# Performance work log

Measured on AMD Instinct MI355X. Metric: run time of the kernel, lower is better.

## Reference

```python
import jax, jax.numpy as jnp
import numpy as np

B, S, D, H = 2, 2048, 256, 8
W_STD = 0.02


def setup_inputs() -> dict:
    key = jax.random.key(0)
    ks = jax.random.split(key, 6)
    x = jax.random.normal(ks[0], (B, S, D), jnp.float32)
    e = jax.random.normal(ks[1], (B, S, D), jnp.float32)
    p = jax.random.normal(ks[2], (B, S, D), jnp.float32)
    W_q = W_STD * jax.random.normal(ks[3], (D, D), jnp.float32)
    W_k = W_STD * jax.random.normal(ks[4], (D, D), jnp.float32)
    W_v = W_STD * jax.random.normal(ks[5], (D, D), jnp.float32)
    gamma = jnp.ones((H, 1, 1), jnp.float32)
    return {"x": x, "e": e, "p": p, "W_q": W_q, "W_k": W_k, "W_v": W_v, "gamma": gamma}


def reference(x, e, p, W_q, W_k, W_v, gamma):
    # use_ppe=True: Q = K = p (broadcast to every head), V = e; each head sees
    # the SAME d_embed-wide copy, so project once and broadcast over heads.
    Q = p @ W_q  # [B,S,D]
    K = p @ W_k  # [B,S,D]
    V = e @ W_v  # [B,S,D]
    # squared euclidean distance (torch.cdist(...,p=2)**2), shared across heads
    q2 = jnp.sum(Q * Q, axis=-1)  # [B,S]
    k2 = jnp.sum(K * K, axis=-1)  # [B,S]
    d2 = q2[:, :, None] + k2[:, None, :] - 2.0 * jnp.einsum('bsd,btd->bst', Q, K)
    d2 = jnp.maximum(d2, 0.0)  # [B,S,S]
    # rbf kernel, per-head gamma: krn = exp(-d2 / (-2*gamma + 1e-6))
    krn = -d2[:, None, :, :] / (-2.0 * gamma + 1e-6)  # [B,H,S,S]
    causal = jnp.tril(jnp.ones((S, S), dtype=bool))  # True where attending allowed
    krn = jnp.where(causal, krn, -jnp.inf)
    krn = jnp.exp(krn)  # masked entries -> exp(-inf) = 0
    # dropout layers run in eval mode (identity)
    out = jnp.einsum('bhst,btd->bhsd', krn, V)  # [B,H,S,D]
    return out
```

## Files before the change

kernel.cpp:

```cpp
#include <hip/hip_runtime.h>
#include <hip/hip_bf16.h>


#define BB   2
#define SS   2048
#define DD   256
#define HH   8
#define BSR  (BB*SS)
#define TSPLIT 4

typedef __bf16 bf16_t;
typedef __bf16 bf16x8 __attribute__((ext_vector_type(8)));
typedef float  f32x4  __attribute__((ext_vector_type(4)));

static __device__ __forceinline__ f32x4 mfma16(bf16x8 a, bf16x8 b, f32x4 c) {
    return __builtin_amdgcn_mfma_f32_16x16x32_bf16(a, b, c, 0, 0, 0);
}

__global__ __launch_bounds__(256) void att_wtrans(
    const float* __restrict__ Wq, const float* __restrict__ Wk,
    const float* __restrict__ Wv,
    bf16_t* __restrict__ WFq_h, bf16_t* __restrict__ WFq_l,
    bf16_t* __restrict__ WFk_h, bf16_t* __restrict__ WFk_l,
    bf16_t* __restrict__ WFv, float* __restrict__ q2, float* __restrict__ k2)
{
    __shared__ float tT[64][68];
    const int tid = threadIdx.x;
    if (blockIdx.x == 48) {
        for (int i = tid; i < BSR; i += 256) { q2[i] = 0.f; k2[i] = 0.f; }
        return;
    }
    const int mat = blockIdx.x >> 4;
    const int tl  = blockIdx.x & 15;
    const int tr  = (tl >> 2) * 64, tc = (tl & 3) * 64;
    const float* W = (mat == 0) ? Wq : ((mat == 1) ? Wk : Wv);

#pragma unroll
    for (int i = 0; i < 4; ++i) {
        const int fidx = i * 256 + tid;
        const int r  = fidx >> 4;
        const int c4 = fidx & 15;
        const float4 v = *(const float4*)(W + (size_t)(tr + r) * DD + tc + c4 * 4);
        tT[c4 * 4 + 0][r] = v.x; tT[c4 * 4 + 1][r] = v.y;
        tT[c4 * 4 + 2][r] = v.z; tT[c4 * 4 + 3][r] = v.w;
    }
    __syncthreads();

#pragma unroll
    for (int i = 0; i < 2; ++i) {
        const int uidx  = i * 256 + tid;
        const int chunk = uidx >> 6;
        const int kc_l  = chunk >> 2, c16 = chunk & 3;
        const int u = uidx & 63, m16 = u & 15, quad = u >> 4;
        const float* src = &tT[c16 * 16 + m16][kc_l * 32 + quad * 8];
        const float4 a = *(const float4*)src;
        const float4 bq = *(const float4*)(src + 4);
        const float f[8] = {a.x, a.y, a.z, a.w, bq.x, bq.y, bq.z, bq.w};
        bf16x8 hi, lo;
#pragma unroll
        for (int j = 0; j < 8; ++j) {
            const bf16_t h = (bf16_t)f[j];
            hi[j] = h; lo[j] = (bf16_t)(f[j] - (float)h);
        }
        const int g16 = (tc >> 4) + c16;
        const int kcg = (tr >> 5) + kc_l;
        const size_t off = ((size_t)(g16 * 8 + kcg)) * 512 + (size_t)u * 8;
        if (mat == 0)      { *(bf16x8*)(WFq_h + off) = hi; *(bf16x8*)(WFq_l + off) = lo; }
        else if (mat == 1) { *(bf16x8*)(WFk_h + off) = hi; *(bf16x8*)(WFk_l + off) = lo; }
        else               { *(bf16x8*)(WFv + off)  = hi; }
    }
}

__global__ __launch_bounds__(256, 2) void att_gemm_qkv(
    const float* __restrict__ p, const float* __restrict__ e,
    const bf16_t* __restrict__ WFq_h, const bf16_t* __restrict__ WFq_l,
    const bf16_t* __restrict__ WFk_h, const bf16_t* __restrict__ WFk_l,
    const bf16_t* __restrict__ WFv,
    bf16_t* __restrict__ QFh, bf16_t* __restrict__ QFl,
    bf16_t* __restrict__ KFh, bf16_t* __restrict__ KFl,
    bf16_t* __restrict__ VF, float* __restrict__ q2, float* __restrict__ k2)
{
    __shared__ float pL[16][264];
    __shared__ float eL[16][264];
    __shared__ float fQ[16][68];
    __shared__ float fK[16][68];
    __shared__ float fV[16][68];

    const int tid  = threadIdx.x;
    const int w    = tid >> 6;
    const int lane = tid & 63;
    const int m16  = lane & 15;
    const int quad = lane >> 4;
    const int row0 = (blockIdx.x >> 2) * 16;
    const int nb   = blockIdx.x & 3;

#pragma unroll
    for (int i = 0; i < 4; ++i) {
        const int fidx = i * 256 + tid;
        const int r  = fidx >> 6;
        const int c4 = fidx & 63;
        const float4 pv = *(const float4*)(p + (size_t)(row0 + r) * DD + c4 * 4);
        const float4 ev = *(const float4*)(e + (size_t)(row0 + r) * DD + c4 * 4);
        *(float4*)&pL[r][c4 * 4] = pv;
        *(float4*)&eL[r][c4 * 4] = ev;
    }
    __syncthreads();

    f32x4 aQ = f32x4{0.f, 0.f, 0.f, 0.f};
    f32x4 aK = f32x4{0.f, 0.f, 0.f, 0.f};
    f32x4 aV = f32x4{0.f, 0.f, 0.f, 0.f};

#pragma unroll 2
    for (int kc = 0; kc < 8; ++kc) {
        const float* ps = &pL[m16][kc * 32 + quad * 8];
        const float* es = &eL[m16][kc * 32 + quad * 8];
        const float4 p0 = *(const float4*)ps;
        const float4 p1 = *(const float4*)(ps + 4);
        const float4 e0 = *(const float4*)es;
        const float4 e1 = *(const float4*)(es + 4);
        const float pa[8] = {p0.x, p0.y, p0.z, p0.w, p1.x, p1.y, p1.z, p1.w};
        const float ea[8] = {e0.x, e0.y, e0.z, e0.w, e1.x, e1.y, e1.z, e1.w};
        bf16x8 aph, apl, aeb;
#pragma unroll
        for (int j = 0; j < 8; ++j) {
            const bf16_t h = (bf16_t)pa[j];
            aph[j] = h;
            apl[j] = (bf16_t)(pa[j] - (float)h);
            aeb[j] = (bf16_t)ea[j];
        }
        const size_t wo = ((size_t)((nb * 4 + w) * 8 + kc)) * 512 + (size_t)lane * 8;
        const bf16x8 bqh = *(const bf16x8*)(WFq_h + wo);
        const bf16x8 bql = *(const bf16x8*)(WFq_l + wo);
        const bf16x8 bkh = *(const bf16x8*)(WFk_h + wo);
        const bf16x8 bkl = *(const bf16x8*)(WFk_l + wo);
        const bf16x8 bv  = *(const bf16x8*)(WFv + wo);
        aQ = mfma16(aph, bqh, aQ);
        aQ = mfma16(apl, bqh, aQ);
        aQ = mfma16(aph, bql, aQ);
        aK = mfma16(aph, bkh, aK);
        aK = mfma16(apl, bkh, aK);
        aK = mfma16(aph, bkl, aK);
        aV = mfma16(aeb, bv, aV);
    }

#pragma unroll
    for (int r = 0; r < 4; ++r) {
        const int rl = quad * 4 + r;
        fQ[rl][w * 16 + m16] = aQ[r];
        fK[rl][w * 16 + m16] = aK[r];
        fV[rl][w * 16 + m16] = aV[r];
    }

#pragma unroll
    for (int r = 0; r < 4; ++r) {
        float vq = aQ[r] * aQ[r], vk = aK[r] * aK[r];
#pragma unroll
        for (int off = 8; off >= 1; off >>= 1) {
            vq += __shfl_xor(vq, off);
            vk += __shfl_xor(vk, off);
        }
        if (m16 == 0) {
            atomicAdd(q2 + row0 + quad * 4 + r, vq);
            atomicAdd(k2 + row0 + quad * 4 + r, vk);
        }
    }

    __syncthreads();

    const int b   = row0 >> 11;
    const int sl  = row0 & 2047;
    const int tt  = sl >> 6;
    const int st  = sl >> 5;
    const int w4  = (sl >> 4) & 3;
    const int mt  = (sl >> 4) & 1;
    const int kc2 = (sl >> 5) & 1;
    const int uh  = (sl >> 4) & 1;

    if (w < 2) {
        const int cl = w;
        const float* src = &fQ[m16][cl * 32 + quad * 8];
        const float4 a = *(const float4*)src;
        const float4 c = *(const float4*)(src + 4);
        const float f[8] = {a.x, a.y, a.z, a.w, c.x, c.y, c.z, c.w};
        bf16x8 hi, lo;
#pragma unroll
        for (int j = 0; j < 8; ++j) {
            const bf16_t h = (bf16_t)f[j];
            hi[j] = h; lo[j] = (bf16_t)(f[j] - (float)h);
        }
        const size_t off = ((size_t)(b * 64 + st)) * 8192
                         + (size_t)(mt * 8 + nb * 2 + cl) * 512 + (size_t)lane * 8;
        *(bf16x8*)(QFh + off) = hi; *(bf16x8*)(QFl + off) = lo;
    } else {
        const int cl = w - 2;
        const float* src = &fK[m16][cl * 32 + quad * 8];
        const float4 a = *(const float4*)src;
        const float4 c = *(const float4*)(src + 4);
        const float f[8] = {a.x, a.y, a.z, a.w, c.x, c.y, c.z, c.w};
        bf16x8 hi, lo;
#pragma unroll
        for (int j = 0; j < 8; ++j) {
            const bf16_t h = (bf16_t)f[j];
            hi[j] = h; lo[j] = (bf16_t)(f[j] - (float)h);
        }
        const size_t off = ((size_t)(b * 32 + tt)) * 16384
                         + (size_t)(w4 * 8 + nb * 2 + cl) * 512 + (size_t)lane * 8;
        *(bf16x8*)(KFh + off) = hi; *(bf16x8*)(KFl + off) = lo;
    }

    if (lane < 32) {
        const int nt  = w;
        const int u   = uh * 32 + lane;
        const int tl0 = (lane >> 4) * 8;
        bf16x8 vb;
#pragma unroll
        for (int j = 0; j < 8; ++j)
            vb[j] = (bf16_t)fV[tl0 + j][nt * 16 + (lane & 15)];
        const size_t off = ((size_t)(b * 32 + tt)) * 16384
                         + (size_t)(nb * 8 + kc2 * 4 + nt) * 512 + (size_t)u * 8;
        *(bf16x8*)(VF + off) = vb;
    }
}

__global__ __launch_bounds__(256, 2) void att_flash(
    const bf16_t* __restrict__ QFh, const bf16_t* __restrict__ QFl,
    const bf16_t* __restrict__ KFh, const bf16_t* __restrict__ KFl,
    const bf16_t* __restrict__ VF, const float* __restrict__ q2,
    const float* __restrict__ k2, const float* __restrict__ gamma,
    float* __restrict__ part, float* __restrict__ out)
{
    __shared__ bf16_t Pb[2][32][72];

    const int tid   = threadIdx.x;
    const int pair  = blockIdx.x >> 3;
    const int sub   = blockIdx.x & 7;
    const int split = sub >> 1;
    const int b     = sub & 1;
    const int wave  = tid >> 6;
    const int lane  = tid & 63;
    const int m16   = lane & 15;
    const int quad  = lane >> 4;

    float g[8];
#pragma unroll
    for (int h = 0; h < 8; ++h) g[h] = gamma[h];

    int pb = 0;

    for (int half = 0; half < 2; ++half) {
        const int st = half ? (63 - pair) : pair;
        const int s0 = st * 32;

        bf16x8 aQh[2][8], aQl[2][8];
        const size_t qtile = ((size_t)(b * 64 + st)) * 8192 + (size_t)lane * 8;
#pragma unroll
        for (int mt = 0; mt < 2; ++mt)
#pragma unroll
            for (int kc = 0; kc < 8; ++kc) {
                const size_t base = qtile + (size_t)(mt * 8 + kc) * 512;
                aQh[mt][kc] = *(const bf16x8*)(QFh + base);
                aQl[mt][kc] = *(const bf16x8*)(QFl + base);
            }

        float q2r[2][4];
#pragma unroll
        for (int mt = 0; mt < 2; ++mt)
#pragma unroll
            for (int r = 0; r < 4; ++r)
                q2r[mt][r] = q2[b * SS + s0 + mt * 16 + quad * 4 + r];

        const int n_tiles = (s0 + 31) / 64 + 1;

        for (int h = 0; h < HH; ++h) {
            int rep = 0;
            while (g[rep] != g[h]) ++rep;
            if (rep != h) continue;
            const float cexp = 1.0f / (2.0f * g[h] - 1e-6f);

            f32x4 O[2][4];
#pragma unroll
            for (int mt = 0; mt < 2; ++mt)
#pragma unroll
                for (int nt = 0; nt < 4; ++nt)
                    O[mt][nt] = f32x4{0.f, 0.f, 0.f, 0.f};

            for (int ti = split; ti < n_tiles; ti += TSPLIT) {
                const int t0 = ti * 64;
                const int tg = t0 + wave * 16 + m16;
                const size_t tile = ((size_t)(b * 32 + ti)) * 16384
                                  + (size_t)wave * 4096 + (size_t)lane * 8;

                bf16x8 vf[2][4];
#pragma unroll
                for (int kc2 = 0; kc2 < 2; ++kc2)
#pragma unroll
                    for (int nt = 0; nt < 4; ++nt)
                        vf[kc2][nt] = *(const bf16x8*)(
                            VF + tile + (size_t)(kc2 * 4 + nt) * 512);
                const float k2v = k2[b * SS + tg];

                f32x4 acc0 = f32x4{0.f, 0.f, 0.f, 0.f};
                f32x4 acc1 = f32x4{0.f, 0.f, 0.f, 0.f};
#pragma unroll
                for (int kc = 0; kc < 8; ++kc) {
                    const bf16x8 bh = *(const bf16x8*)(KFh + tile + (size_t)kc * 512);
                    const bf16x8 bl = *(const bf16x8*)(KFl + tile + (size_t)kc * 512);
                    acc0 = mfma16(aQh[0][kc], bh, acc0);
                    acc1 = mfma16(aQh[1][kc], bh, acc1);
                    acc0 = mfma16(aQl[0][kc], bh, acc0);
                    acc1 = mfma16(aQl[1][kc], bh, acc1);
                    acc0 = mfma16(aQh[0][kc], bl, acc0);
                    acc1 = mfma16(aQh[1][kc], bl, acc1);
                }

#pragma unroll
                for (int mt = 0; mt < 2; ++mt) {
#pragma unroll
                    for (int r = 0; r < 4; ++r) {
                        const int sl = mt * 16 + quad * 4 + r;
                        const int sg = s0 + sl;
                        const float dotv = mt ? acc1[r] : acc0[r];
                        float d2 = q2r[mt][r] + k2v - 2.0f * dotv;
                        d2 = fmaxf(d2, 0.0f);
                        const float wgt = (tg <= sg) ? __expf(cexp * d2) : 0.0f;
                        Pb[pb][sl][wave * 16 + m16] = (bf16_t)wgt;
                    }
                }
                __syncthreads();

#pragma unroll
                for (int kc2 = 0; kc2 < 2; ++kc2) {
                    const bf16x8 pa0 = *(const bf16x8*)&Pb[pb][m16][kc2 * 32 + quad * 8];
                    const bf16x8 pa1 = *(const bf16x8*)&Pb[pb][m16 + 16][kc2 * 32 + quad * 8];
#pragma unroll
                    for (int nt = 0; nt < 4; ++nt) {
                        O[0][nt] = mfma16(pa0, vf[kc2][nt], O[0][nt]);
                        O[1][nt] = mfma16(pa1, vf[kc2][nt], O[1][nt]);
                    }
                }
                pb ^= 1;
            }

            float* dst = (split == 0)
                ? out  + (((size_t)b * HH + h) * SS + s0) * DD
                : part + ((((size_t)(split - 1) * BB + b) * HH + h) * SS + s0) * DD;
#pragma unroll
            for (int mt = 0; mt < 2; ++mt)
#pragma unroll
                for (int nt = 0; nt < 4; ++nt)
#pragma unroll
                    for (int r = 0; r < 4; ++r)
                        dst[(size_t)(mt * 16 + quad * 4 + r) * DD
                            + wave * 64 + nt * 16 + m16] = O[mt][nt][r];
        }
    }
}

__global__ __launch_bounds__(256) void att_reduce_bcast(
    const float* __restrict__ gamma, const float* __restrict__ part,
    float* __restrict__ out)
{
    const int j = blockIdx.x * 256 + threadIdx.x;
    const int b = blockIdx.y;
    const int slab = SS * DD / 4;

    float g[8];
#pragma unroll
    for (int h = 0; h < 8; ++h) g[h] = gamma[h];

    const float4* pp = (const float4*)part;
    float4* o4 = (float4*)out;

    float4 repval{0.f, 0.f, 0.f, 0.f};
    int last_rep = -1;
#pragma unroll
    for (int h = 0; h < HH; ++h) {
        int rep = 0;
        while (g[rep] != g[h]) ++rep;
        float4* o = o4 + ((size_t)(b * HH + h)) * slab + j;
        if (rep == h) {
            float4 v = *o;
#pragma unroll
            for (int k = 0; k < 3; ++k) {
                const float4 pv = pp[(((size_t)k * BB + b) * HH + h) * slab + j];
                v.x += pv.x; v.y += pv.y; v.z += pv.z; v.w += pv.w;
            }
            *o = v; repval = v; last_rep = h;
        } else {
            if (last_rep != rep) {
                repval = o4[((size_t)(b * HH + rep)) * slab + j];
                last_rep = rep;
            }
            *o = repval;
        }
    }
}

extern "C" void kernel_launch(void* const* d_in, const int* in_sizes, int n_in,
                              void* d_out, int out_size, void* d_ws, size_t ws_size,
                              hipStream_t stream) {
    (void)in_sizes; (void)n_in; (void)out_size; (void)ws_size;
    const float* e     = (const float*)d_in[1];
    const float* p     = (const float*)d_in[2];
    const float* Wq    = (const float*)d_in[3];
    const float* Wk    = (const float*)d_in[4];
    const float* Wv    = (const float*)d_in[5];
    const float* gamma = (const float*)d_in[6];

    const size_t NROW = (size_t)BSR * DD;
    bf16_t* WFq_h = (bf16_t*)d_ws;
    bf16_t* WFq_l = WFq_h + DD * DD;
    bf16_t* WFk_h = WFq_l + DD * DD;
    bf16_t* WFk_l = WFk_h + DD * DD;
    bf16_t* WFv   = WFk_l + DD * DD;
    float*  q2    = (float*)(WFv + DD * DD);
    float*  k2    = q2 + BSR;
    bf16_t* QFh   = (bf16_t*)(k2 + BSR);
    bf16_t* QFl   = QFh + NROW;
    bf16_t* KFh   = QFl + NROW;
    bf16_t* KFl   = KFh + NROW;
    bf16_t* VF    = KFl + NROW;
    float*  part  = (float*)(VF + NROW);

    float* out = (float*)d_out;

    att_wtrans<<<dim3(49), dim3(256), 0, stream>>>(
        Wq, Wk, Wv, WFq_h, WFq_l, WFk_h, WFk_l, WFv, q2, k2);

    att_gemm_qkv<<<dim3((BSR / 16) * 4), dim3(256), 0, stream>>>(
        p, e, WFq_h, WFq_l, WFk_h, WFk_l, WFv, QFh, QFl, KFh, KFl, VF, q2, k2);

    att_flash<<<dim3(32 * TSPLIT * BB), dim3(256), 0, stream>>>(
        QFh, QFl, KFh, KFl, VF, q2, k2, gamma, part, out);

    att_reduce_bcast<<<dim3(SS * DD / 4 / 256, BB), dim3(256), 0, stream>>>(
        gamma, part, out);
}
```

Before: 136.1 us.

## Double-buffer K tiles via async global-to-LDS loads and prefetch V in flash kernel

The flash kernel now streams the next K tile (hi and lo parts) into a double-buffered 64KB LDS region with global_load_lds, and prefetches the next V fragments into a second register slot while computing scores for the current tile. The three split-bf16 dot-product chains get independent accumulators to shorten MFMA dependency chains. The aim is to hide global-load latency behind MFMA work. In exchange, the large LDS footprint and launch_bounds(256,1) limit the kernel to one block per CU, and correctness relies on the barrier waiting for the async LDS loads. The QKV GEMM block-index mapping is also remapped to group rows per XCD, with occupancy hint raised to 3.

```diff
diff --git a/kernel.cpp b/kernel.cpp
--- a/kernel.cpp
+++ b/kernel.cpp
@@ -15,6 +15,13 @@
 
 static __device__ __forceinline__ f32x4 mfma16(bf16x8 a, bf16x8 b, f32x4 c) {
     return __builtin_amdgcn_mfma_f32_16x16x32_bf16(a, b, c, 0, 0, 0);
+}
+
+static __device__ __forceinline__ void gld_lds16(const bf16_t* g, bf16_t* l) {
+    __builtin_amdgcn_global_load_lds(
+        (const __attribute__((address_space(1))) unsigned int*)(unsigned long long)g,
+        (__attribute__((address_space(3))) unsigned int*)(unsigned int)(unsigned long long)l,
+        16, 0, 0);
 }
 
 __global__ __launch_bounds__(256) void att_wtrans(
@@ -71,7 +78,7 @@
     }
 }
 
-__global__ __launch_bounds__(256, 2) void att_gemm_qkv(
+__global__ __launch_bounds__(256, 3) void att_gemm_qkv(
     const float* __restrict__ p, const float* __restrict__ e,
     const bf16_t* __restrict__ WFq_h, const bf16_t* __restrict__ WFq_l,
     const bf16_t* __restrict__ WFk_h, const bf16_t* __restrict__ WFk_l,
@@ -91,8 +98,10 @@
     const int lane = tid & 63;
     const int m16  = lane & 15;
     const int quad = lane >> 4;
-    const int row0 = (blockIdx.x >> 2) * 16;
-    const int nb   = blockIdx.x & 3;
+    const int xcd  = blockIdx.x & 7;
+    const int jid  = blockIdx.x >> 3;
+    const int nb   = jid >> 5;
+    const int row0 = (xcd * 32 + (jid & 31)) * 16;
 
 #pragma unroll
     for (int i = 0; i < 4; ++i) {
@@ -222,13 +231,14 @@
     }
 }
 
-__global__ __launch_bounds__(256, 2) void att_flash(
+__global__ __launch_bounds__(256, 1) void att_flash(
     const bf16_t* __restrict__ QFh, const bf16_t* __restrict__ QFl,
     const bf16_t* __restrict__ KFh, const bf16_t* __restrict__ KFl,
     const bf16_t* __restrict__ VF, const float* __restrict__ q2,
     const float* __restrict__ k2, const float* __restrict__ gamma,
     float* __restrict__ part, float* __restrict__ out)
 {
+    __shared__ bf16_t Klds[2][2][16384];
     __shared__ bf16_t Pb[2][32][72];
 
     const int tid   = threadIdx.x;
@@ -245,8 +255,6 @@
 #pragma unroll
     for (int h = 0; h < 8; ++h) g[h] = gamma[h];
 
-    int pb = 0;
-
     for (int half = 0; half < 2; ++half) {
         const int st = half ? (63 - pair) : pair;
         const int s0 = st * 32;
@@ -284,62 +292,102 @@
                 for (int nt = 0; nt < 4; ++nt)
                     O[mt][nt] = f32x4{0.f, 0.f, 0.f, 0.f};
 
-            for (int ti = split; ti < n_tiles; ti += TSPLIT) {
-                const int t0 = ti * 64;
-                const int tg = t0 + wave * 16 + m16;
-                const size_t tile = ((size_t)(b * 32 + ti)) * 16384
+            bf16x8 vf[2][2][4];
+
+            auto DMA_K = [&](int tiX, int par) {
+                const size_t tb = ((size_t)(b * 32 + tiX)) * 16384
+                                + (size_t)wave * 4096 + (size_t)lane * 8;
+#pragma unroll
+                for (int i = 0; i < 8; ++i) {
+                    gld_lds16(KFh + tb + (size_t)i * 512,
+                              &Klds[par][0][wave * 4096 + i * 512]);
+                    gld_lds16(KFl + tb + (size_t)i * 512,
+                              &Klds[par][1][wave * 4096 + i * 512]);
+                }
+            };
+
+            auto LOADV = [&](int tiX, int slot) {
+                const size_t tile = ((size_t)(b * 32 + tiX)) * 16384
                                   + (size_t)wave * 4096 + (size_t)lane * 8;
-
-                bf16x8 vf[2][4];
 #pragma unroll
                 for (int kc2 = 0; kc2 < 2; ++kc2)
 #pragma unroll
                     for (int nt = 0; nt < 4; ++nt)
-                        vf[kc2][nt] = *(const bf16x8*)(
+                        vf[slot][kc2][nt] = *(const bf16x8*)(
                             VF + tile + (size_t)(kc2 * 4 + nt) * 512);
+            };
+
+            auto SCORES = [&](int tiX, int par, int pb) {
+                const int tg = tiX * 64 + wave * 16 + m16;
                 const float k2v = k2[b * SS + tg];
-
-                f32x4 acc0 = f32x4{0.f, 0.f, 0.f, 0.f};
-                f32x4 acc1 = f32x4{0.f, 0.f, 0.f, 0.f};
+                f32x4 hh0 = f32x4{0.f, 0.f, 0.f, 0.f};
+                f32x4 hh1 = f32x4{0.f, 0.f, 0.f, 0.f};
+                f32x4 lh0 = f32x4{0.f, 0.f, 0.f, 0.f};
+                f32x4 lh1 = f32x4{0.f, 0.f, 0.f, 0.f};
+                f32x4 hl0 = f32x4{0.f, 0.f, 0.f, 0.f};
+                f32x4 hl1 = f32x4{0.f, 0.f, 0.f, 0.f};
 #pragma unroll
                 for (int kc = 0; kc < 8; ++kc) {
-                    const bf16x8 bh = *(const bf16x8*)(KFh + tile + (size_t)kc * 512);
-                    const bf16x8 bl = *(const bf16x8*)(KFl + tile + (size_t)kc * 512);
-                    acc0 = mfma16(aQh[0][kc], bh, acc0);
-                    acc1 = mfma16(aQh[1][kc], bh, acc1);
-                    acc0 = mfma16(aQl[0][kc], bh, acc0);
-                    acc1 = mfma16(aQl[1][kc], bh, acc1);
-                    acc0 = mfma16(aQh[0][kc], bl, acc0);
-                    acc1 = mfma16(aQh[1][kc], bl, acc1);
+                    const bf16x8 bh = *(const bf16x8*)
+                        &Klds[par][0][wave * 4096 + kc * 512 + lane * 8];
+                    const bf16x8 bl = *(const bf16x8*)
+                        &Klds[par][1][wave * 4096 + kc * 512 + lane * 8];
+                    hh0 = mfma16(aQh[0][kc], bh, hh0);
+                    hh1 = mfma16(aQh[1][kc], bh, hh1);
+                    lh0 = mfma16(aQl[0][kc], bh, lh0);
+                    lh1 = mfma16(aQl[1][kc], bh, lh1);
+                    hl0 = mfma16(aQh[0][kc], bl, hl0);
+                    hl1 = mfma16(aQh[1][kc], bl, hl1);
                 }
-
 #pragma unroll
                 for (int mt = 0; mt < 2; ++mt) {
 #pragma unroll
                     for (int r = 0; r < 4; ++r) {
                         const int sl = mt * 16 + quad * 4 + r;
                         const int sg = s0 + sl;
-                        const float dotv = mt ? acc1[r] : acc0[r];
+                        const float dotv = mt ? (hh1[r] + lh1[r] + hl1[r])
+                                              : (hh0[r] + lh0[r] + hl0[r]);
                         float d2 = q2r[mt][r] + k2v - 2.0f * dotv;
                         d2 = fmaxf(d2, 0.0f);
-                        const float wgt = (tg <= sg) ? __expf(cexp * d2) : 0.0f;
-                        Pb[pb][sl][wave * 16 + m16] = (bf16_t)wgt;
+                        Pb[pb][sl][wave * 16 + m16] =
+                            (bf16_t)((tg <= sg) ? __expf(cexp * d2) : 0.0f);
                     }
                 }
-                __syncthreads();
-
+            };
+
+            auto PV = [&](int pb, int slot) {
 #pragma unroll
                 for (int kc2 = 0; kc2 < 2; ++kc2) {
-                    const bf16x8 pa0 = *(const bf16x8*)&Pb[pb][m16][kc2 * 32 + quad * 8];
-                    const bf16x8 pa1 = *(const bf16x8*)&Pb[pb][m16 + 16][kc2 * 32 + quad * 8];
+                    const bf16x8 pa0 = *(const bf16x8*)
+                        &Pb[pb][m16][kc2 * 32 + quad * 8];
+                    const bf16x8 pa1 = *(const bf16x8*)
+                        &Pb[pb][m16 + 16][kc2 * 32 + quad * 8];
 #pragma unroll
                     for (int nt = 0; nt < 4; ++nt) {
-                        O[0][nt] = mfma16(pa0, vf[kc2][nt], O[0][nt]);
-                        O[1][nt] = mfma16(pa1, vf[kc2][nt], O[1][nt]);
+                        O[0][nt] = mfma16(pa0, vf[slot][kc2][nt], O[0][nt]);
+                        O[1][nt] = mfma16(pa1, vf[slot][kc2][nt], O[1][nt]);
                     }
                 }
-                pb ^= 1;
+            };
+
+            int ti = split;
+            if (ti < n_tiles) {
+                DMA_K(ti, 0);
+                LOADV(ti, 0);
+                __syncthreads();
+                int par = 0, pb = 0, slot = 0;
+                while (true) {
+                    const int tn = ti + TSPLIT;
+                    const bool more = (tn < n_tiles);
+                    if (more) { DMA_K(tn, par ^ 1); LOADV(tn, slot ^ 1); }
+                    SCORES(ti, par, pb);
+                    __syncthreads();
+                    PV(pb, slot);
+                    if (!more) break;
+                    ti = tn; par ^= 1; pb ^= 1; slot ^= 1;
+                }
             }
+            __syncthreads();
 
             float* dst = (split == 0)
                 ? out  + (((size_t)b * HH + h) * SS + s0) * DD
@@ -381,7 +429,7 @@
         if (rep == h) {
             float4 v = *o;
 #pragma unroll
-            for (int k = 0; k < 3; ++k) {
+            for (int k = 0; k < TSPLIT - 1; ++k) {
                 const float4 pv = pp[(((size_t)k * BB + b) * HH + h) * slab + j];
                 v.x += pv.x; v.y += pv.y; v.z += pv.z; v.w += pv.w;
             }
```

Result: slower. 150.1 us (+10.3%).
